# Kernel optimization log

Measured on AMD Instinct MI355X. Metric: run time of the kernel, lower is better.

## Reference

```python
import jax, jax.numpy as jnp
import numpy as np
from jax import lax

# config (mirrors KeypointExtract init)
NMS_DIST = 4
CONF_THRESH = 0.015
CELL = 8
BORDER = 4
KPT_NUM = 1024
WINDOW_SIZE = 5
TEMP_INIT = 10.0
MAX_CAND = 8192  # fixed candidate budget (top-scoring pixels fed to greedy NMS)


def _make_offsets():
    # linspace(-(ws//2), ws//2, ws//2*2+1) meshgrid -> (R,2) integer offsets (dy, dx)
    lin = np.linspace(-(WINDOW_SIZE // 2), WINDOW_SIZE // 2, num=WINDOW_SIZE // 2 * 2 + 1)
    o0, o1 = np.meshgrid(lin, lin)
    off = np.concatenate([o0.reshape(-1, 1), o1.reshape(-1, 1)], axis=1)
    return jnp.asarray(off.astype(np.int32))  # (R,2)


def depth2space(semi):
    # softmax over 65 channels, drop dustbin, pixel-shuffle 8x8 cells to full res
    dense = jax.nn.softmax(semi, axis=1)
    nodust = dense[:, :-1, :, :]                      # (B,64,Hc,Wc)
    B, C, Hc, Wc = nodust.shape
    cell = CELL
    hm = nodust.transpose(0, 2, 3, 1).reshape(B, Hc, Wc, cell, cell)
    hm = hm.transpose(0, 1, 3, 2, 4).reshape(B, Hc * cell, Wc * cell)
    return hm                                         # (B,H,W)


def greedy_nms(ys, xs, valid, H, W, pad):
    # faithful greedy grid-suppression NMS: candidates arrive sorted by conf desc
    w = 2 * pad + 1
    grid0 = jnp.zeros((H + 2 * pad, W + 2 * pad), dtype=bool)  # True = suppressed

    def step(grid, inp):
        y, x, v = inp
        keep = v & jnp.logical_not(grid[y + pad, x + pad])
        patch = lax.dynamic_slice(grid, (y, x), (w, w))
        grid = lax.dynamic_update_slice(grid, jnp.logical_or(patch, keep), (y, x))
        return grid, keep

    _, kept = lax.scan(step, grid0, (ys, xs, valid))
    return kept


def grid_sample_bilinear(img, gx, gy):
    # torch F.grid_sample, mode=bilinear, padding=zeros, align_corners=False
    B, C, Hc, Wc = img.shape
    ix = (gx + 1.0) * (Wc / 2.0) - 0.5
    iy = (gy + 1.0) * (Hc / 2.0) - 0.5
    x0 = jnp.floor(ix); y0 = jnp.floor(iy)
    wx1 = ix - x0; wy1 = iy - y0
    bidx = jnp.arange(B)[:, None]

    def tap(xi, yi):
        inb = (xi >= 0) & (xi < Wc) & (yi >= 0) & (yi < Hc)
        xc = jnp.clip(xi, 0, Wc - 1).astype(jnp.int32)
        yc = jnp.clip(yi, 0, Hc - 1).astype(jnp.int32)
        v = img[bidx, :, yc, xc]                      # (B,N,C)
        return jnp.where(inb[..., None], v, 0.0)

    v00 = tap(x0, y0); v01 = tap(x0 + 1, y0)
    v10 = tap(x0, y0 + 1); v11 = tap(x0 + 1, y0 + 1)
    w00 = ((1 - wx1) * (1 - wy1))[..., None]
    w01 = (wx1 * (1 - wy1))[..., None]
    w10 = ((1 - wx1) * wy1)[..., None]
    w11 = (wx1 * wy1)[..., None]
    out = v00 * w00 + v01 * w01 + v10 * w10 + v11 * w11  # (B,N,C)
    return out.transpose(0, 2, 1)                        # (B,C,N)


def setup_inputs() -> dict:
    key = jax.random.key(0)
    k1, k2 = jax.random.split(key)
    semi = jax.random.normal(k1, (4, 65, 120, 160), dtype=jnp.float32)
    coarse_desc = jax.random.normal(k2, (4, 256, 120, 160), dtype=jnp.float32)
    temp = jnp.ones((1,), dtype=jnp.float32) * TEMP_INIT
    return {"semi": semi, "coarse_desc": coarse_desc, "temp": temp}


def reference(semi, coarse_desc, temp):
    heatmap = depth2space(semi)                       # (B,H,W)
    B, H, W = heatmap.shape
    offs = _make_offsets()                            # (R,2) = (dy,dx)
    R = offs.shape[0]

    # ---- keypoint detection (no-grad in original) ----
    hm_sg = lax.stop_gradient(heatmap)
    vals, idx = lax.top_k(hm_sg.reshape(B, -1), MAX_CAND)   # sorted conf desc
    ys = (idx // W).astype(jnp.int32)
    xs = (idx % W).astype(jnp.int32)
    valid = vals >= CONF_THRESH
    kept = jax.vmap(lambda y, x, v: greedy_nms(y, x, v, H, W, NMS_DIST))(ys, xs, valid)
    border_ok = (xs >= BORDER) & (xs < W - BORDER) & (ys >= BORDER) & (ys < H - BORDER)
    sel_key = jnp.where(kept & border_ok, vals, -jnp.inf)
    _, sel = lax.top_k(sel_key, KPT_NUM)              # top kpt_num survivors by conf
    ysel = jnp.take_along_axis(ys, sel, axis=1)       # (B,N)
    xsel = jnp.take_along_axis(xs, sel, axis=1)

    # ---- spatial soft-argmax (differentiable) ----
    yy = ysel[:, None, :] + offs[None, :, 0:1]        # (B,R,N)
    xx = xsel[:, None, :] + offs[None, :, 1:2]
    bidx = jnp.arange(B)[:, None, None]
    region = heatmap[bidx, yy, xx]                    # (B,R,N) gather
    attn = jax.nn.softmax(region * temp[0], axis=1)
    offs_f = offs.astype(jnp.float32)
    dy = jnp.einsum('brn,r->bn', attn, offs_f[:, 0])
    dx = jnp.einsum('brn,r->bn', attn, offs_f[:, 1])
    y_f = ysel.astype(jnp.float32) + dy
    x_f = xsel.astype(jnp.float32) + dx
    batch_pts = jnp.stack([x_f, y_f], axis=-1)        # (B,N,2) (x,y)

    # ---- descriptor sampling ----
    gx = x_f / (W / 2.0) - 1.0
    gy = y_f / (H / 2.0) - 1.0
    desc = grid_sample_bilinear(coarse_desc, gx, gy)  # (B,C,N)
    desc = desc / jnp.maximum(jnp.linalg.norm(desc, axis=1, keepdims=True), 1e-12)
    return batch_pts, desc, heatmap
```

## Files before the change

kernel.cpp:

```cpp
#include <hip/hip_runtime.h>
#include <cstdint>

typedef unsigned int u32;
typedef unsigned long long u64;
typedef unsigned short u16;
typedef unsigned char u8;

#define HM_H 960
#define HM_W 1280
#define HM_N (HM_H*HM_W)
#define BATCH 4
#define CAND 8192
#define KPT 1024
#define NCELL 19200

#define WS_HISTA 0x0
#define WS_HISTB 0x100000
#define WS_META  0x200000
#define WS_CAND  0x200400
#define WS_EQ    0x240400
#define WS_SIDX  0x260400
#define WS_SEL   0x280400
#define WS_CM    0x284400
#define WS_CS    0x2CF400
#define WS_SPOT  0x365400
#define WS_BST   0x385400
#define WS_BLST  0x398040
#define WS_CNT   0x3A8040
#define WS_STAT  0x3C8040
#define WS_CLST  0x3D0040
#define WS_CAND2 0x4D0040


__device__ inline double pixval64(const float* __restrict__ semi, const float* __restrict__ cm,
                                  const double* __restrict__ cs, int b, u32 idx){
  u32 y = idx / HM_W, x = idx - y*HM_W;
  u32 hc = y>>3, wc = x>>3, ch = ((y&7)<<3) | (x&7);
  float logit = semi[(((size_t)b*65 + ch)*120 + hc)*160 + wc];
  int cid = b*NCELL + (int)(hc*160 + wc);
  return exp((double)logit - (double)cm[cid]) / cs[cid];
}

__global__ __launch_bounds__(256) void k_heatmap(const float* __restrict__ semi, float* __restrict__ hm,
                          float* __restrict__ cm, double* __restrict__ cs){
  int tid = blockIdx.x*256 + threadIdx.x;
  if (tid >= BATCH*NCELL*8) return;
  int cell = tid >> 3, sub = tid & 7;
  int wc = cell % 160; int hc = (cell/160) % 120; int b = cell / NCELL;
  const float* p = semi + (size_t)b*65*NCELL + hc*160 + wc;
  float r[8];
  #pragma unroll
  for (int i=0;i<8;i++) r[i] = p[(size_t)(sub*8+i)*NCELL];
  float extra = (sub==7) ? p[(size_t)64*NCELL] : -3.0e38f;
  float m = extra;
  #pragma unroll
  for (int i=0;i<8;i++) m = fmaxf(m, r[i]);
  m = fmaxf(m, __shfl_xor(m,1,64));
  m = fmaxf(m, __shfl_xor(m,2,64));
  m = fmaxf(m, __shfl_xor(m,4,64));
  double S = 0.0;
  #pragma unroll
  for (int i=0;i<8;i++) S += exp((double)r[i] - (double)m);
  if (sub==7) S += exp((double)extra - (double)m);
  S += __shfl_xor(S,1,64);
  S += __shfl_xor(S,2,64);
  S += __shfl_xor(S,4,64);
  if (sub==0){ cm[cell]=m; cs[cell]=S; }
  float* out = hm + ((size_t)b*HM_H + hc*8 + sub)*HM_W + wc*8;
  float o[8];
  #pragma unroll
  for (int i=0;i<8;i++) o[i] = (float)(exp((double)r[i] - (double)m) / S);
  *reinterpret_cast<float4*>(out)     = make_float4(o[0],o[1],o[2],o[3]);
  *reinterpret_cast<float4*>(out + 4) = make_float4(o[4],o[5],o[6],o[7]);
}

#define HBIN0 0x3C75u
#define NHBIN 780
__global__ void k_histA(const float* __restrict__ hm, u32* __restrict__ hist){
  __shared__ u32 lh[NHBIN];
  int b = blockIdx.x >> 8;
  int chunk = blockIdx.x & 255;
  for (int i=threadIdx.x;i<NHBIN;i+=256) lh[i]=0;
  __syncthreads();
  const u32 FLOOR = 0x3C75C28Fu;
  const float4* src = (const float4*)(hm + (size_t)b*HM_N);
  int per = (HM_N/4)/256;
  int start = chunk*per;
  for (int i=start+(int)threadIdx.x; i<start+per; i+=256){
    float4 v = src[i];
    u32 bs;
    bs=__float_as_uint(v.x); if (bs>=FLOOR){ u32 bi=(bs>>16)-HBIN0; if(bi>=NHBIN)bi=NHBIN-1; atomicAdd(&lh[bi],1u); }
    bs=__float_as_uint(v.y); if (bs>=FLOOR){ u32 bi=(bs>>16)-HBIN0; if(bi>=NHBIN)bi=NHBIN-1; atomicAdd(&lh[bi],1u); }
    bs=__float_as_uint(v.z); if (bs>=FLOOR){ u32 bi=(bs>>16)-HBIN0; if(bi>=NHBIN)bi=NHBIN-1; atomicAdd(&lh[bi],1u); }
    bs=__float_as_uint(v.w); if (bs>=FLOOR){ u32 bi=(bs>>16)-HBIN0; if(bi>=NHBIN)bi=NHBIN-1; atomicAdd(&lh[bi],1u); }
  }
  __syncthreads();
  u32* h = hist + b*65536 + HBIN0;
  for (int i=threadIdx.x;i<NHBIN;i+=256){
    u32 c=lh[i]; if (c) atomicAdd(&h[i], c);
  }
}

__global__ void k_histB(const float* __restrict__ hm, const u32* __restrict__ meta, u32* __restrict__ hist){
  const u32 FLOOR = 0x3C75C28Fu;
  u32 nv = BATCH*HM_N/4;
  for (u32 i = blockIdx.x*blockDim.x + threadIdx.x; i < nv; i += gridDim.x*blockDim.x){
    float4 v = reinterpret_cast<const float4*>(hm)[i];
    u32 b = (i*4) / HM_N;
    u32 piv = meta[b*64+0];
    u32* h = hist + b*65536;
    u32 bs;
    bs = __float_as_uint(v.x); if (bs >= FLOOR && (bs>>16)==piv) atomicAdd(&h[bs & 0xFFFFu], 1u);
    bs = __float_as_uint(v.y); if (bs >= FLOOR && (bs>>16)==piv) atomicAdd(&h[bs & 0xFFFFu], 1u);
    bs = __float_as_uint(v.z); if (bs >= FLOOR && (bs>>16)==piv) atomicAdd(&h[bs & 0xFFFFu], 1u);
    bs = __float_as_uint(v.w); if (bs >= FLOOR && (bs>>16)==piv) atomicAdd(&h[bs & 0xFFFFu], 1u);
  }
}

__global__ void k_reduce(const u32* __restrict__ hist, u32* __restrict__ meta, int phase){
  int b = blockIdx.x;
  const u32* h = hist + b*65536;
  u32* mb = meta + b*64;
  u32 K = (phase==0) ? (u32)CAND : mb[1];
  int t = threadIdx.x;
  __shared__ u32 suf[1024];
  u32 s = 0;
  for (int i=0;i<64;i++) s += h[t*64+i];
  suf[t]=s; __syncthreads();
  for (int off=1; off<1024; off<<=1){
    u32 add = (t+off<1024) ? suf[t+off] : 0u;
    u32 nv2 = suf[t] + add;
    __syncthreads();
    suf[t]=nv2; __syncthreads();
  }
  u32 total = suf[0];
  u32 cumAbove = (t<1023) ? suf[t+1] : 0u;
  bool found = (cumAbove < K) && (cumAbove + s >= K);
  if (found){
    u32 cum = cumAbove; int bin = 0; u32 cA = cumAbove;
    for (int i=63;i>=0;i--){
      u32 c = h[t*64+i];
      if (cum + c >= K){ bin = t*64+i; cA = cum; break; }
      cum += c;
    }
    if (phase==0){ mb[0]=(u32)bin; mb[2]=cA; mb[1]=K-cA; }
    else {
      u32 V = (mb[0]<<16) | (u32)bin; mb[3]=V;
      u32 cg = mb[2] + cA; mb[4]=cg;
      mb[5] = (cg < (u32)CAND) ? ((u32)CAND - cg) : 0u;
    }
  }
  if (t==0 && total < K){
    if (phase==0){ mb[0]=0; mb[2]=total; mb[1]=K-total; }
    else {
      u32 V = (mb[0]<<16); mb[3]=V;
      u32 cg = mb[2] + total; mb[4]=cg;
      mb[5] = (cg < (u32)CAND) ? ((u32)CAND - cg) : 0u;
    }
  }
}

#define CB_CAP 4800
__global__ __launch_bounds__(256) void k_compact(const float* __restrict__ hm, u32* __restrict__ meta,
                          u64* __restrict__ cand, u32* __restrict__ eq){
  __shared__ u32 pixb[CB_CAP];
  __shared__ u32 bsb[CB_CAP];
  __shared__ u32 eqb[CB_CAP];
  __shared__ u32 cnt, ecnt, gbase, ebase;
  int b = blockIdx.x >> 8;
  int chunk = blockIdx.x & 255;
  if (threadIdx.x==0){ cnt=0u; ecnt=0u; }
  __syncthreads();
  u32 V = meta[b*64+3];
  const float4* src = (const float4*)(hm + (size_t)b*HM_N);
  int per = (HM_N/4)/256;
  int start = chunk*per;
  for (int i=start+(int)threadIdx.x; i<start+per; i+=256){
    float4 v = src[i];
    u32 pix = (u32)i*4u;
    u32 bs4[4];
    bs4[0]=__float_as_uint(v.x); bs4[1]=__float_as_uint(v.y);
    bs4[2]=__float_as_uint(v.z); bs4[3]=__float_as_uint(v.w);
    #pragma unroll
    for (int c2=0;c2<4;c2++){
      u32 bs = bs4[c2];
      if (bs > V){ u32 p = atomicAdd(&cnt,1u); pixb[p]=pix+(u32)c2; bsb[p]=bs; }
      else if (bs == V){ u32 e = atomicAdd(&ecnt,1u); eqb[e]=pix+(u32)c2; }
    }
  }
  __syncthreads();
  if (threadIdx.x==0){
    gbase = cnt  ? atomicAdd(&meta[b*64+6], cnt)  : 0u;
    ebase = ecnt ? atomicAdd(&meta[b*64+7], ecnt) : 0u;
  }
  __syncthreads();
  u32 c0=cnt, e0=ecnt, gb=gbase, eb=ebase;
  for (u32 i=threadIdx.x; i<c0; i+=256){
    u32 s2 = gb+i;
    if (s2 < CAND) cand[(size_t)b*CAND+s2] = (((u64)(~bsb[i]))<<32)|(u64)pixb[i];
  }
  for (u32 i=threadIdx.x; i<e0; i+=256){
    u32 s2 = eb+i;
    if (s2 < CAND) eq[(size_t)b*CAND+s2] = eqb[i];
  }
}

__global__ void k_eqprep(const u32* __restrict__ meta, u64* __restrict__ cand, const u32* __restrict__ eq,
                         const float* __restrict__ semi, const float* __restrict__ cm,
                         const double* __restrict__ cs){
  int b = blockIdx.x;
  __shared__ double vv[64];
  __shared__ u32 ii[64];
  if (threadIdx.x != 0) return;
  const u32* mb = meta + b*64;
  u32 countGt = mb[4], needEq = mb[5], V32 = mb[3];
  int n = (int)mb[7]; if (n > 64) n = 64;
  for (int j=0;j<n;j++){
    ii[j] = eq[(size_t)b*CAND + j];
    vv[j] = pixval64(semi, cm, cs, b, ii[j]);
  }
  for (int j=1;j<n;j++){
    double vj = vv[j]; u32 ij = ii[j];
    int q = j-1;
    while (q >= 0 && (vv[q] < vj || (vv[q] == vj && ii[q] > ij))){
      vv[q+1]=vv[q]; ii[q+1]=ii[q]; q--;
    }
    vv[q+1]=vj; ii[q+1]=ij;
  }
  u64 vq = ((u64)(~V32))<<32;
  for (u32 r=0; r<needEq; r++){
    u64 key = (r < (u32)n) ? (vq | (u64)ii[r]) : ~0ull;
    if (countGt + r < CAND) cand[(size_t)b*CAND + countGt + r] = key;
  }
}

__global__ __launch_bounds__(512,1) void k_sortloc(u64* __restrict__ cand){
  __shared__ u64 sk[2048];
  int blk = blockIdx.x;
  int b = blk >> 2, seg = blk & 3;
  int t = threadIdx.x;
  int lane = t & 63, w = t >> 6;
  int base = w*256 + lane;
  u64* cb = cand + (size_t)b*CAND + seg*2048;
  u64 E[4];
  #pragma unroll
  for (int m=0;m<4;m++) E[m] = cb[base + m*64];

  for (int k2=2; k2<=2048; k2<<=1){
    int j = k2>>1;
    if (j >= 256){
      __syncthreads();
      #pragma unroll
      for (int m=0;m<4;m++) sk[base + m*64] = E[m];
      __syncthreads();
      for (; j>=256; j>>=1){
        int lj = __ffs(j)-1;
        for (int p=t; p<1024; p+=512){
          int i = ((p >> lj) << (lj+1)) | (p & (j-1));
          int l = i | j;
          bool up = ((i & k2)==0);
          u64 a=sk[i], c=sk[l];
          if ((a>c)==up){ sk[i]=c; sk[l]=a; }
        }
        __syncthreads();
      }
      #pragma unroll
      for (int m=0;m<4;m++) E[m] = sk[base + m*64];
      j = 128;
    }
    for (; j>=64; j>>=1){
      int mm = j>>6;
      #pragma unroll
      for (int m=0;m<4;m++){
        if ((m & mm)==0){
          int i = base + m*64;
          bool up = ((i & k2)==0);
          u64 a=E[m], c=E[m|mm];
          if ((a>c)==up){ E[m]=c; E[m|mm]=a; }
        }
      }
    }
    for (; j>=1; j>>=1){
      bool low0 = ((lane & j)==0);
      #pragma unroll
      for (int m=0;m<4;m++){
        int i = base + m*64;
        bool up = ((i & k2)==0);
        bool keepmin = (low0==up);
        u64 P = (u64)__shfl_xor((long long)E[m], j, 64);
        u64 mn = E[m]<P ? E[m] : P;
        u64 mx = E[m]<P ? P : E[m];
        E[m] = keepmin ? mn : mx;
      }
    }
  }
  #pragma unroll
  for (int m=0;m<4;m++) cb[base + m*64] = E[m];
}

__global__ __launch_bounds__(256) void k_merge(const u64* __restrict__ src, u64* __restrict__ dst, int L){
  int tid = blockIdx.x*256 + (int)threadIdx.x;
  if (tid >= BATCH*CAND) return;
  int b = tid >> 13;
  int e = tid & (CAND-1);
  int pairBase = (e / (2*L)) * (2*L);
  int off = e - pairBase;
  const u64* A = src + ((size_t)b<<13) + pairBase;
  const u64* B = A + L;
  bool inA = off < L;
  int i = inA ? off : off - L;
  u64 key = inA ? A[i] : B[i];
  const u64* O = inA ? B : A;
  int lo = 0, hi = L;
  if (inA){
    while (lo < hi){ int mid=(lo+hi)>>1; if (O[mid] < key) lo=mid+1; else hi=mid; }
  } else {
    while (lo < hi){ int mid=(lo+hi)>>1; if (O[mid] <= key) lo=mid+1; else hi=mid; }
  }
  dst[((size_t)b<<13) + pairBase + i + lo] = key;
}

__global__ __launch_bounds__(1024,1) void k_sortfix(const u64* __restrict__ cand, u32* __restrict__ sidx,
                       const float* __restrict__ semi, const float* __restrict__ cm,
                       const double* __restrict__ cs){
  int b = blockIdx.x;
  extern __shared__ u64 sk[];
  int t = threadIdx.x;
  const u64* cb = cand + (size_t)b*CAND;
  for (int i=t;i<CAND;i+=1024) sk[i]=cb[i];
  __syncthreads();
  for (int pass=0; pass<8; pass++){
    int par = pass & 1;
    for (int q=t; q<CAND/2; q+=1024){
      int p = par + 2*q;
      if (p+1 < CAND){
        u64 a = sk[p], c = sk[p+1];
        u32 ha = (u32)(a>>32), hc2 = (u32)(c>>32);
        if (ha == hc2 && ha != 0xFFFFFFFFu){
          double va = pixval64(semi, cm, cs, b, (u32)a);
          double vc = pixval64(semi, cm, cs, b, (u32)c);
          if (va < vc || (va == vc && (u32)a > (u32)c)){ sk[p]=c; sk[p+1]=a; }
        }
      }
    }
    __syncthreads();
  }
  for (int i=t;i<CAND;i+=1024) sidx[(size_t)b*CAND+i] = (u32)sk[i];
}

#define NBX 80
#define NBY 60
#define NBK (NBX*NBY)
#define BSTSTRIDE 4804
__global__ __launch_bounds__(1024) void k_nbuild(const u32* __restrict__ sidx, u32* __restrict__ spot,
                                                 u32* __restrict__ bstG, u16* __restrict__ blistG){
  __shared__ u32 bcnt[NBK];
  __shared__ u32 bst[NBK];
  __shared__ u32 tsum[1024];
  int b = blockIdx.x, t = threadIdx.x;
  const u32* sb = sidx + (size_t)b*CAND;
  for (int i=t;i<NBK;i+=1024) bcnt[i]=0;
  __syncthreads();
  for (int r=t;r<CAND;r+=1024){
    u32 idx = sb[r];
    u32 p;
    if (idx != 0xFFFFFFFFu){
      u32 y = idx/HM_W, x = idx - y*HM_W;
      p = (y<<16)|x;
      atomicAdd(&bcnt[(y>>4)*NBX+(x>>4)], 1u);
    } else p = 0xFFFFFFFFu;
    spot[(size_t)b*CAND+r] = p;
  }
  __syncthreads();
  u32 lsum=0;
  int base5 = t*5;
  if (base5 < NBK){
    #pragma unroll
    for (int j2=0;j2<5;j2++){ int ix=base5+j2; if (ix<NBK) lsum += bcnt[ix]; }
  }
  tsum[t]=lsum;
  __syncthreads();
  for (int off=1; off<1024; off<<=1){
    u32 add = (t>=off)? tsum[t-off] : 0u;
    __syncthreads();
    tsum[t] += add;
    __syncthreads();
  }
  if (base5 < NBK){
    u32 run = (t==0)?0u:tsum[t-1];
    #pragma unroll
    for (int j2=0;j2<5;j2++){
      int ix=base5+j2; if (ix<NBK){ u32 c=bcnt[ix]; bst[ix]=run; run+=c; }
    }
  }
  __syncthreads();
  for (int i=t;i<NBK;i+=1024){ bcnt[i]=bst[i]; bstG[(size_t)b*BSTSTRIDE+i]=bst[i]; }
  if (t==0) bstG[(size_t)b*BSTSTRIDE+NBK] = tsum[1023];
  __syncthreads();
  for (int r=t;r<CAND;r+=1024){
    u32 p = spot[(size_t)b*CAND+r];
    if (p != 0xFFFFFFFFu){
      u32 bu = ((p>>16)>>4)*NBX + ((p&0xFFFFu)>>4);
      u32 slot = atomicAdd(&bcnt[bu],1u);
      blistG[(size_t)b*CAND+slot] = (u16)r;
    }
  }
}

#define CLCAP 12
__global__ __launch_bounds__(256) void k_nconf(const u32* __restrict__ spot, const u32* __restrict__ bstG,
                                               const u16* __restrict__ blistG, u32* __restrict__ cntG,
                                               u8* __restrict__ statG, u16* __restrict__ clistG){
  int b = blockIdx.x >> 5;
  int r = (blockIdx.x & 31)*256 + (int)threadIdx.x;
  const u32* sp = spot + (size_t)b*CAND;
  u32 p = sp[r];
  if (p == 0xFFFFFFFFu){ statG[(size_t)b*CAND+r]=2; return; }
  int y=(int)(p>>16), x=(int)(p&0xFFFFu);
  int by=y>>4, bx=x>>4;
  const u32* bs = bstG + (size_t)b*BSTSTRIDE;
  const u16* bl = blistG + (size_t)b*CAND;
  u16* cl = clistG + ((size_t)b*CAND + r)*CLCAP;
  int cnt=0; bool heavy=false;
  for (int dy=-1; dy<=1; dy++){
    int yy=by+dy; if (yy<0||yy>=NBY) continue;
    for (int dx=-1; dx<=1; dx++){
      int xx=bx+dx; if (xx<0||xx>=NBX) continue;
      int bu=yy*NBX+xx;
      int s=(int)bs[bu], e=(int)bs[bu+1];
      for (int q=s;q<e;q++){
        int j = (int)bl[q];
        if (j >= r) continue;
        u32 pj = sp[j];
        int ady = y-(int)(pj>>16); ady = ady<0?-ady:ady;
        int adx = x-(int)(pj&0xFFFFu); adx = adx<0?-adx:adx;
        if (ady<=4 && adx<=4){
          if (cnt < CLCAP) cl[cnt++] = (u16)j;
          else heavy = true;
        }
      }
    }
  }
  if (heavy){ cntG[(size_t)b*CAND+r]=0xFFFFFFFFu; statG[(size_t)b*CAND+r]=0; }
  else { cntG[(size_t)b*CAND+r]=(u32)cnt; statG[(size_t)b*CAND+r] = (cnt==0)?1:0; }
}

__global__ __launch_bounds__(1024,1) void k_nresolve(const u32* __restrict__ spot, const u32* __restrict__ bstG,
                                                     const u16* __restrict__ blistG, const u32* __restrict__ cntG,
                                                     u8* __restrict__ statG, const u16* __restrict__ clistG,
                                                     u32* __restrict__ sel){
  __shared__ u8 sstat[CAND];
  __shared__ u16 wl[2][CAND];
  __shared__ u32 wcnt[2];
  __shared__ u32 wpass[256];
  __shared__ u32 wpre[256];
  int b = blockIdx.x, t = threadIdx.x;
  const u32* sp = spot + (size_t)b*CAND;
  if (t<2) wcnt[t]=0;
  __syncthreads();
  for (int r=t;r<CAND;r+=1024){
    u8 st = statG[(size_t)b*CAND+r];
    sstat[r]=st;
    if (st==0){ u32 w=atomicAdd(&wcnt[0],1u); wl[0][w]=(u16)r; }
  }
  __syncthreads();
  int cur=0;
  for (int round=0; round<8192; ++round){
    int n = (int)wcnt[cur];
    if (n==0) break;
    int nx = cur^1;
    for (int i=t;i<n;i+=1024){
      int r = (int)wl[cur][i];
      u32 c = cntG[(size_t)b*CAND+r];
      bool supp=false, blocked=false;
      if (c==0xFFFFFFFFu){
        u32 p = sp[r];
        int y=(int)(p>>16), x=(int)(p&0xFFFFu);
        int by=y>>4, bx=x>>4;
        const u32* bs = bstG + (size_t)b*BSTSTRIDE;
        const u16* bl = blistG + (size_t)b*CAND;
        for (int dy=-1; dy<=1 && !supp; dy++){
          int yy=by+dy; if (yy<0||yy>=NBY) continue;
          for (int dx=-1; dx<=1 && !supp; dx++){
            int xx=bx+dx; if (xx<0||xx>=NBX) continue;
            int bu=yy*NBX+xx;
            int s=(int)bs[bu], e=(int)bs[bu+1];
            for (int q=s;q<e;q++){
              int j = (int)bl[q];
              if (j >= r) continue;
              u32 pj = sp[j];
              int ady = y-(int)(pj>>16); ady = ady<0?-ady:ady;
              int adx = x-(int)(pj&0xFFFFu); adx = adx<0?-adx:adx;
              if (ady<=4 && adx<=4){
                u8 st = sstat[j];
                if (st==1){ supp=true; break; }
                if (st==0) blocked=true;
              }
            }
          }
        }
      } else {
        const u16* cl = clistG + ((size_t)b*CAND + r)*CLCAP;
        for (u32 k=0;k<c;k++){
          u8 st = sstat[cl[k]];
          if (st==1){ supp=true; break; }
          if (st==0) blocked=true;
        }
      }
      if (supp) sstat[r]=2;
      else if (!blocked) sstat[r]=1;
      else { u32 w=atomicAdd(&wcnt[nx],1u); wl[nx][w]=(u16)r; }
    }
    __syncthreads();
    if (t==0) wcnt[cur]=0;
    cur = nx;
    __syncthreads();
  }

  if (t < 256){
    u32 w = 0;
    for (int bi2=0;bi2<32;bi2++){
      int r = t*32+bi2;
      if (sstat[r]==1){
        u32 p = sp[r];
        u32 y=p>>16, x=p&0xFFFFu;
        if (x>=4 && x<HM_W-4 && y>=4 && y<HM_H-4) w |= (1u<<bi2);
      }
    }
    wpass[t]=w;
    wpre[t]=__popc(w);
  }
  __syncthreads();
  for (int off=1; off<256; off<<=1){
    u32 add = 0;
    if (t<256 && t>=off) add = wpre[t-off];
    __syncthreads();
    if (t<256) wpre[t] += add;
    __syncthreads();
  }
  u32 P = wpre[255];
  for (int r=t;r<CAND;r+=1024){
    u32 word = wpass[r>>5];
    u32 bit = (u32)r & 31u;
    bool pass = (word>>bit)&1u;
    u32 prank = ((r>>5)>0 ? wpre[(r>>5)-1] : 0u) + __popc(word & ((1u<<bit)-1u));
    u32 p = sp[r];
    u32 y,x;
    if (p==0xFFFFFFFFu){ y=HM_H-1; x=HM_W-1; } else { y=p>>16; x=p&0xFFFFu; }
    if (pass){
      if (prank < KPT) sel[b*KPT+prank] = (y<<16)|x;
    } else {
      u32 frank = (u32)r - prank;
      u32 slot = P + frank;
      if (slot < KPT) sel[b*KPT+slot] = (y<<16)|x;
    }
  }
}

__global__ void k_refine(const u32* __restrict__ sel, const float* __restrict__ hm,
                         const float* __restrict__ temp, float* __restrict__ pts){
  int t = blockIdx.x*256 + threadIdx.x;
  if (t >= BATCH*KPT) return;
  int b = t >> 10;
  u32 p = sel[t];
  int y = (int)(p>>16), x = (int)(p & 0xFFFFu);
  float T = temp[0];
  const float* hb = hm + (size_t)b*HM_N;
  float r[25]; float m = -3.0e38f;
  #pragma unroll
  for (int i=0;i<25;i++){
    int yy = y + (i%5) - 2;
    int xx = x + (i/5) - 2;
    if (yy<0) yy += HM_H; if (yy<0) yy=0; if (yy>HM_H-1) yy=HM_H-1;
    if (xx<0) xx += HM_W; if (xx<0) xx=0; if (xx>HM_W-1) xx=HM_W-1;
    float v = hb[yy*HM_W+xx] * T;
    r[i]=v; m=fmaxf(m,v);
  }
  float s=0.f, dy=0.f, dx=0.f;
  #pragma unroll
  for (int i=0;i<25;i++){
    float e = expf(r[i]-m);
    s += e;
    dy += e * (float)((i%5)-2);
    dx += e * (float)((i/5)-2);
  }
  dy /= s; dx /= s;
  pts[t*2+0] = (float)x + dx;
  pts[t*2+1] = (float)y + dy;
}

__global__ void k_desc(const float* __restrict__ pts, const float* __restrict__ cd, float* __restrict__ desc){
  int blk = blockIdx.x;
  int b = blk >> 10; int n = blk & 1023;
  int c = threadIdx.x;
  float xf = pts[blk*2+0], yf = pts[blk*2+1];
  float gx = xf/640.0f - 1.0f;
  float gy = yf/480.0f - 1.0f;
  float ix = (gx+1.0f)*80.0f - 0.5f;
  float iy = (gy+1.0f)*60.0f - 0.5f;
  float x0f = floorf(ix), y0f = floorf(iy);
  float wx1 = ix-x0f, wy1 = iy-y0f;
  int x0=(int)x0f, y0=(int)y0f;
  const float* base = cd + ((size_t)b*256 + c)*NCELL;
  bool xi0 = (x0>=0)&&(x0<160), xi1 = (x0+1>=0)&&(x0+1<160);
  bool yi0 = (y0>=0)&&(y0<120), yi1 = (y0+1>=0)&&(y0+1<120);
  int xc0 = min(max(x0,0),159),   xc1 = min(max(x0+1,0),159);
  int yc0 = min(max(y0,0),119),   yc1 = min(max(y0+1,0),119);
  float v00=0.f,v01=0.f,v10=0.f,v11=0.f;
  if (xi0&&yi0) v00 = base[yc0*160+xc0];
  if (xi1&&yi0) v01 = base[yc0*160+xc1];
  if (xi0&&yi1) v10 = base[yc1*160+xc0];
  if (xi1&&yi1) v11 = base[yc1*160+xc1];
  float out = v00*(1.f-wx1)*(1.f-wy1) + v01*wx1*(1.f-wy1)
            + v10*(1.f-wx1)*wy1      + v11*wx1*wy1;
  float ss = out*out;
  #pragma unroll
  for (int off=32; off>=1; off>>=1) ss += __shfl_down(ss, off);
  __shared__ float red[4];
  if ((c&63)==0) red[c>>6] = ss;
  __syncthreads();
  float tot = red[0]+red[1]+red[2]+red[3];
  float nrm = fmaxf(sqrtf(tot), 1e-12f);
  desc[((size_t)b*256 + c)*1024 + n] = out / nrm;
}

extern "C" void kernel_launch(void* const* d_in, const int* in_sizes, int n_in,
                              void* d_out, int out_size, void* d_ws, size_t ws_size,
                              hipStream_t stream){
  const float* semi = (const float*)d_in[0];
  const float* cdsc = (const float*)d_in[1];
  const float* temp = (const float*)d_in[2];
  float* pts  = (float*)d_out;
  float* desc = pts + 4*1024*2;
  float* hm   = desc + (size_t)4*256*1024;
  char* ws = (char*)d_ws;
  u32* histA = (u32*)(ws + WS_HISTA);
  u32* histB = (u32*)(ws + WS_HISTB);
  u32* meta  = (u32*)(ws + WS_META);
  u64* cand  = (u64*)(ws + WS_CAND);
  u32* eq    = (u32*)(ws + WS_EQ);
  u32* sidx  = (u32*)(ws + WS_SIDX);
  u32* sel   = (u32*)(ws + WS_SEL);
  float*  cm = (float*)(ws + WS_CM);
  double* cs = (double*)(ws + WS_CS);
  u32* spot  = (u32*)(ws + WS_SPOT);
  u32* bstG  = (u32*)(ws + WS_BST);
  u16* blistG= (u16*)(ws + WS_BLST);
  u32* cntG  = (u32*)(ws + WS_CNT);
  u8*  statG = (u8*)(ws + WS_STAT);
  u16* clistG= (u16*)(ws + WS_CLST);
  u64* cand2 = (u64*)(ws + WS_CAND2);

  hipMemsetAsync(ws, 0, WS_CAND, stream);

  k_heatmap<<<2400, 256, 0, stream>>>(semi, hm, cm, cs);
  k_histA  <<<1024, 256, 0, stream>>>(hm, histA);
  k_reduce <<<4, 1024, 0, stream>>>(histA, meta, 0);
  k_histB  <<<1024, 256, 0, stream>>>(hm, meta, histB);
  k_reduce <<<4, 1024, 0, stream>>>(histB, meta, 1);
  k_compact<<<1024, 256, 0, stream>>>(hm, meta, cand, eq);
  k_eqprep <<<4, 64, 0, stream>>>(meta, cand, eq, semi, cm, cs);
  k_sortloc<<<16, 512, 0, stream>>>(cand);
  k_merge  <<<128, 256, 0, stream>>>(cand, cand2, 2048);
  k_merge  <<<128, 256, 0, stream>>>(cand2, cand, 4096);
  hipFuncSetAttribute((const void*)k_sortfix, hipFuncAttributeMaxDynamicSharedMemorySize, CAND*8);
  k_sortfix<<<4, 1024, CAND*8, stream>>>(cand, sidx, semi, cm, cs);
  k_nbuild <<<4, 1024, 0, stream>>>(sidx, spot, bstG, blistG);
  k_nconf  <<<128, 256, 0, stream>>>(spot, bstG, blistG, cntG, statG, clistG);
  k_nresolve<<<4, 1024, 0, stream>>>(spot, bstG, blistG, cntG, statG, clistG, sel);
  k_refine <<<16, 256, 0, stream>>>(sel, hm, temp, pts);
  k_desc   <<<4096, 256, 0, stream>>>(pts, cdsc, desc);
}
```

Measured before the change: 223.1 us.

## Stage descriptor planes in LDS per channel and split normalization kernel

Descriptor sampling now assigns one block per (batch, channel) plane, copies the full coarse descriptor plane into shared memory with vectorized loads, then bilinearly samples all keypoints from LDS and writes coalesced outputs. L2 normalization across channels moves to a separate tiled kernel that reads, reduces and rescales the descriptor tiles. The aim is to replace scattered global gathers and strided stores with streaming reads, at the cost of reading the whole descriptor tensor, a large LDS footprint limiting occupancy, and an extra launch.

```diff
diff --git a/kernel.cpp b/kernel.cpp
--- a/kernel.cpp
+++ b/kernel.cpp
@@ -589,39 +589,79 @@
   pts[t*2+1] = (float)y + dy;
 }
 
-__global__ void k_desc(const float* __restrict__ pts, const float* __restrict__ cd, float* __restrict__ desc){
+__global__ __launch_bounds__(256) void k_desc1(const float* __restrict__ pts, const float* __restrict__ cd,
+                                               float* __restrict__ desc){
+  extern __shared__ float plane[];
   int blk = blockIdx.x;
-  int b = blk >> 10; int n = blk & 1023;
-  int c = threadIdx.x;
-  float xf = pts[blk*2+0], yf = pts[blk*2+1];
-  float gx = xf/640.0f - 1.0f;
-  float gy = yf/480.0f - 1.0f;
-  float ix = (gx+1.0f)*80.0f - 0.5f;
-  float iy = (gy+1.0f)*60.0f - 0.5f;
-  float x0f = floorf(ix), y0f = floorf(iy);
-  float wx1 = ix-x0f, wy1 = iy-y0f;
-  int x0=(int)x0f, y0=(int)y0f;
-  const float* base = cd + ((size_t)b*256 + c)*NCELL;
-  bool xi0 = (x0>=0)&&(x0<160), xi1 = (x0+1>=0)&&(x0+1<160);
-  bool yi0 = (y0>=0)&&(y0<120), yi1 = (y0+1>=0)&&(y0+1<120);
-  int xc0 = min(max(x0,0),159),   xc1 = min(max(x0+1,0),159);
-  int yc0 = min(max(y0,0),119),   yc1 = min(max(y0+1,0),119);
-  float v00=0.f,v01=0.f,v10=0.f,v11=0.f;
-  if (xi0&&yi0) v00 = base[yc0*160+xc0];
-  if (xi1&&yi0) v01 = base[yc0*160+xc1];
-  if (xi0&&yi1) v10 = base[yc1*160+xc0];
-  if (xi1&&yi1) v11 = base[yc1*160+xc1];
-  float out = v00*(1.f-wx1)*(1.f-wy1) + v01*wx1*(1.f-wy1)
-            + v10*(1.f-wx1)*wy1      + v11*wx1*wy1;
-  float ss = out*out;
-  #pragma unroll
-  for (int off=32; off>=1; off>>=1) ss += __shfl_down(ss, off);
-  __shared__ float red[4];
-  if ((c&63)==0) red[c>>6] = ss;
-  __syncthreads();
-  float tot = red[0]+red[1]+red[2]+red[3];
-  float nrm = fmaxf(sqrtf(tot), 1e-12f);
-  desc[((size_t)b*256 + c)*1024 + n] = out / nrm;
+  int b = blk >> 8;
+  const float4* s4 = (const float4*)(cd + (size_t)blk*NCELL);
+  float4* p4 = (float4*)plane;
+  for (int i=threadIdx.x; i<NCELL/4; i+=256) p4[i]=s4[i];
+  __syncthreads();
+  for (int n=threadIdx.x; n<KPT; n+=256){
+    float xf = pts[(b*KPT+n)*2+0], yf = pts[(b*KPT+n)*2+1];
+    float gx = xf/640.0f - 1.0f;
+    float gy = yf/480.0f - 1.0f;
+    float ix = (gx+1.0f)*80.0f - 0.5f;
+    float iy = (gy+1.0f)*60.0f - 0.5f;
+    float x0f = floorf(ix), y0f = floorf(iy);
+    float wx1 = ix-x0f, wy1 = iy-y0f;
+    int x0=(int)x0f, y0=(int)y0f;
+    bool xi0 = (x0>=0)&&(x0<160), xi1 = (x0+1>=0)&&(x0+1<160);
+    bool yi0 = (y0>=0)&&(y0<120), yi1 = (y0+1>=0)&&(y0+1<120);
+    int xc0 = min(max(x0,0),159),   xc1 = min(max(x0+1,0),159);
+    int yc0 = min(max(y0,0),119),   yc1 = min(max(y0+1,0),119);
+    float v00 = (xi0&&yi0) ? plane[yc0*160+xc0] : 0.f;
+    float v01 = (xi1&&yi0) ? plane[yc0*160+xc1] : 0.f;
+    float v10 = (xi0&&yi1) ? plane[yc1*160+xc0] : 0.f;
+    float v11 = (xi1&&yi1) ? plane[yc1*160+xc1] : 0.f;
+    float out = v00*(1.f-wx1)*(1.f-wy1) + v01*wx1*(1.f-wy1)
+              + v10*(1.f-wx1)*wy1      + v11*wx1*wy1;
+    desc[(size_t)blk*KPT + n] = out;
+  }
+}
+
+#define DN_T 32
+__global__ __launch_bounds__(256) void k_dnorm(float* __restrict__ desc){
+  __shared__ float tile[256*DN_T];
+  __shared__ float part[8*DN_T];
+  __shared__ float nrm[DN_T];
+  int b = blockIdx.x >> 5;
+  int n0 = (blockIdx.x & 31)*DN_T;
+  int t = threadIdx.x;
+  float* db = desc + (size_t)b*256*KPT + n0;
+  for (int k=0;k<8;k++){
+    int idx = t + 256*k;
+    int c = idx >> 3, f4 = idx & 7;
+    float4 v = *reinterpret_cast<const float4*>(db + (size_t)c*KPT + f4*4);
+    *reinterpret_cast<float4*>(&tile[c*DN_T + f4*4]) = v;
+  }
+  __syncthreads();
+  {
+    int n = t & (DN_T-1), q = t >> 5;
+    float s = 0.f;
+    #pragma unroll
+    for (int k=0;k<32;k++){
+      float v = tile[(q+8*k)*DN_T + n];
+      s += v*v;
+    }
+    part[q*DN_T + n] = s;
+  }
+  __syncthreads();
+  if (t < DN_T){
+    float tot = 0.f;
+    #pragma unroll
+    for (int q=0;q<8;q++) tot += part[q*DN_T + t];
+    nrm[t] = fmaxf(sqrtf(tot), 1e-12f);
+  }
+  __syncthreads();
+  for (int k=0;k<8;k++){
+    int idx = t + 256*k;
+    int c = idx >> 3, f4 = idx & 7;
+    float4 v = *reinterpret_cast<const float4*>(&tile[c*DN_T + f4*4]);
+    v.x /= nrm[f4*4+0]; v.y /= nrm[f4*4+1]; v.z /= nrm[f4*4+2]; v.w /= nrm[f4*4+3];
+    *reinterpret_cast<float4*>(db + (size_t)c*KPT + f4*4) = v;
+  }
 }
 
 extern "C" void kernel_launch(void* const* d_in, const int* in_sizes, int n_in,
@@ -669,5 +709,7 @@
   k_nconf  <<<128, 256, 0, stream>>>(spot, bstG, blistG, cntG, statG, clistG);
   k_nresolve<<<4, 1024, 0, stream>>>(spot, bstG, blistG, cntG, statG, clistG, sel);
   k_refine <<<16, 256, 0, stream>>>(sel, hm, temp, pts);
-  k_desc   <<<4096, 256, 0, stream>>>(pts, cdsc, desc);
-}
+  hipFuncSetAttribute((const void*)k_desc1, hipFuncAttributeMaxDynamicSharedMemorySize, NCELL*4);
+  k_desc1  <<<1024, 256, NCELL*4, stream>>>(pts, cdsc, desc);
+  k_dnorm  <<<128, 256, 0, stream>>>(desc);
+}
```

Measured after the change: 200.5 us. 1.11x faster.
